# Kernel optimization log

Hardware: AMD Instinct MI355X
Metric: run time of the kernel (lower is better)

## Reference

```python
import jax, jax.numpy as jnp
import numpy as np

NUM_JOINTS = 24
IN_DIM = 256      # PoseMLP hidden_dim (per-joint input feature)
HID = 128         # MLP default hidden_dim
OUT_DIM = 6
B = 16384

def setup_inputs() -> dict:
    key = jax.random.key(0)
    ks = jax.random.split(key, 7)
    s1 = 1.0 / np.sqrt(IN_DIM)   # torch Linear init scale (uniform bound)
    s2 = 1.0 / np.sqrt(HID)
    return {
        "pose_feat": jax.random.normal(ks[0], (B, NUM_JOINTS, IN_DIM), dtype=jnp.float32),
        # stacked per-joint weights: Linear stores W as (out, in); we keep (in, out)
        "W1": jax.random.uniform(ks[1], (NUM_JOINTS, IN_DIM, HID), minval=-s1, maxval=s1, dtype=jnp.float32),
        "b1": jax.random.uniform(ks[2], (NUM_JOINTS, HID), minval=-s1, maxval=s1, dtype=jnp.float32),
        "W2": jax.random.uniform(ks[3], (NUM_JOINTS, HID, HID), minval=-s2, maxval=s2, dtype=jnp.float32),
        "b2": jax.random.uniform(ks[4], (NUM_JOINTS, HID), minval=-s2, maxval=s2, dtype=jnp.float32),
        "W3": jax.random.uniform(ks[5], (NUM_JOINTS, HID, OUT_DIM), minval=-s2, maxval=s2, dtype=jnp.float32),
        "b3": jax.random.uniform(ks[6], (NUM_JOINTS, OUT_DIM), minval=-s2, maxval=s2, dtype=jnp.float32),
    }

def reference(pose_feat, W1, b1, W2, b2, W3, b3):
    # Batched per-joint MLPs (fuses the 24 independent small MLPs into 3 grouped GEMMs)
    h = jax.nn.relu(jnp.einsum('bji,jih->bjh', pose_feat, W1) + b1)  # [B,24,128]
    h = jax.nn.relu(jnp.einsum('bjh,jhk->bjk', h, W2) + b2)          # [B,24,128]
    out = jnp.einsum('bjh,jho->bjo', h, W3) + b3                     # [B,24,6]
    return out
```

## Files before the change

kernel.cpp:

```cpp
#include <hip/hip_runtime.h>
#include <hip/hip_fp16.h>

typedef _Float16 half_t;
typedef __attribute__((ext_vector_type(8))) _Float16 half8;
typedef __attribute__((ext_vector_type(4))) _Float16 half4;
typedef __attribute__((ext_vector_type(4))) float floatx4;

#define NJ 24
#define IN_DIM 256
#define HID 128
#define OUT_DIM 6
#define BATCH 16384

#define NBJ 10
#define GRID (NJ * NBJ)
#define TPJ (BATCH / 16)
#define SLOTS (NBJ * 16)

#define W1_JSTRIDE (8 * 128 * 32)
#define W2_JSTRIDE (4 * 128 * 32)
#define W3_JSTRIDE (16 * 128)
#define WT1_ELEMS (NJ * W1_JSTRIDE)
#define WT2_ELEMS (NJ * W2_JSTRIDE)
#define WT3_ELEMS (NJ * W3_JSTRIDE)
#define WT2_OFF WT1_ELEMS
#define WT3_OFF (WT1_ELEMS + WT2_ELEMS)
#define B3P_BYTE_OFF ((size_t)(WT1_ELEMS + WT2_ELEMS + WT3_ELEMS) * 2)
#define PREP_TOTAL (WT1_ELEMS + WT2_ELEMS + WT3_ELEMS + NJ * 16)

__global__ void posemlp_prep(const float* __restrict__ W1, const float* __restrict__ W2,
                             const float* __restrict__ W3, const float* __restrict__ b3,
                             half_t* __restrict__ wt, float* __restrict__ b3p) {
    int t = blockIdx.x * 256 + threadIdx.x;
    if (t < WT1_ELEMS) {
        int j = t / W1_JSTRIDE, r = t % W1_JSTRIDE;
        int ks = r / 4096, r2 = r % 4096;
        int n = r2 / 32, kk = r2 % 32, k = ks * 32 + kk;
        wt[t] = (half_t)W1[((size_t)j * IN_DIM + k) * HID + n];
    } else if (t < WT2_OFF + WT2_ELEMS) {
        int u = t - WT2_OFF;
        int j = u / W2_JSTRIDE, r = u % W2_JSTRIDE;
        int ks = r / 4096, r2 = r % 4096;
        int n = r2 / 32, kk = r2 % 32, k = ks * 32 + kk;
        wt[t] = (half_t)W2[((size_t)j * HID + k) * HID + n];
    } else if (t < WT3_OFF + WT3_ELEMS) {
        int u = t - WT3_OFF;
        int j = u / W3_JSTRIDE, r = u % W3_JSTRIDE;
        int n = r / 128, k = r % 128;
        wt[t] = (n < OUT_DIM) ? (half_t)W3[((size_t)j * HID + k) * OUT_DIM + n] : (half_t)0.0f;
    } else if (t < PREP_TOTAL) {
        int u = t - WT3_OFF - WT3_ELEMS;
        int j = u / 16, n = u % 16;
        b3p[u] = (n < OUT_DIM) ? b3[j * OUT_DIM + n] : 0.0f;
    }
}

__device__ inline void gll16(const void* g, void* l) {
    __builtin_amdgcn_global_load_lds(
        (const __attribute__((address_space(1))) unsigned int*)g,
        (__attribute__((address_space(3))) unsigned int*)l, 16, 0, 0);
}

__device__ inline half8 lds_read8(const half_t* base, int r, int k) {
    int byte = r * 256 + k * 2;
    byte ^= (r & 7) << 4;
    return *(const half8*)((const char*)base + byte);
}
__device__ inline void lds_write4(half_t* base, int r, int n, half4 v) {
    int byte = r * 256 + n * 2;
    byte ^= (r & 7) << 4;
    *(half4*)((char*)base + byte) = v;
}

__device__ inline half8 cvt8(floatx4 a, floatx4 b) {
    half8 h;
    h[0] = (_Float16)a[0]; h[1] = (_Float16)a[1]; h[2] = (_Float16)a[2]; h[3] = (_Float16)a[3];
    h[4] = (_Float16)b[0]; h[5] = (_Float16)b[1]; h[6] = (_Float16)b[2]; h[7] = (_Float16)b[3];
    return h;
}

__global__ __launch_bounds__(1024) void posemlp_main(
    const float* __restrict__ X, const half_t* __restrict__ wt,
    const float* __restrict__ b1, const float* __restrict__ b2,
    const float* __restrict__ b3p, float* __restrict__ out) {
    __shared__ half_t lds[81920];

    const int bid0 = blockIdx.x;
    const int bid = (bid0 & 7) * 30 + (bid0 >> 3);
    const int j = bid / NBJ, bw = bid % NBJ;
    const int tid = threadIdx.x;
    const int wv = tid >> 6;
    const int l = tid & 63;
    const int lrow = l & 15;
    const int q = l >> 4;

    const half_t* w1j = wt + (size_t)j * W1_JSTRIDE;
    const half_t* w2j = wt + WT2_OFF + (size_t)j * W2_JSTRIDE;
    const half_t* w3j = wt + WT3_OFF + (size_t)j * W3_JSTRIDE;

    const int s = bw * 16 + wv;
    const int nt = (TPJ - s + SLOTS - 1) / SLOTS;

    const float* xg = X + ((size_t)(s * 16 + lrow) * NJ + j) * IN_DIM + q * 8;

    floatx4 px[4][2];
#pragma unroll
    for (int c = 0; c < 4; ++c) {
        px[c][0] = *(const floatx4*)(xg + c * 32);
        px[c][1] = *(const floatx4*)(xg + c * 32 + 4);
    }

    if (wv < 8) {
        const int n = tid >> 2, ss2 = tid & 3;
        const int srcoff = n * 32 + (ss2 ^ ((n >> 1) & 3)) * 8;
#pragma unroll
        for (int c = 0; c < 8; ++c)
            gll16(w1j + c * 4096 + srcoff, &lds[c * 4096 + wv * 512]);
#pragma unroll
        for (int c = 0; c < 4; ++c)
            gll16(w2j + c * 4096 + srcoff, &lds[32768 + c * 4096 + wv * 512]);
    }

    half8 a3[4];
#pragma unroll
    for (int ks = 0; ks < 4; ++ks)
        a3[ks] = *(const half8*)&w3j[lrow * 128 + (ks * 4 + q) * 8];

    half_t* scr = &lds[49152 + wv * 2048];

    __syncthreads();

    for (int i = 0; i < nt; ++i) {
        const size_t nstep = (i + 1 < nt) ? (size_t)(SLOTS * 16) * NJ * IN_DIM : 0;

        floatx4 acc[8] = {};
#pragma unroll
        for (int ks = 0; ks < 8; ++ks) {
            half8 bx = cvt8(px[ks & 3][0], px[ks & 3][1]);
            {
                const float* p = (ks < 4) ? (xg + (ks + 4) * 32)
                                          : (xg + nstep + (ks - 4) * 32);
                px[ks & 3][0] = *(const floatx4*)(p);
                px[ks & 3][1] = *(const floatx4*)(p + 4);
            }
#pragma unroll
            for (int nf = 0; nf < 8; ++nf) {
                const int n = nf * 16 + lrow;
                half8 a = *(const half8*)&lds[ks * 4096 + n * 32 + (q ^ ((n >> 1) & 3)) * 8];
                acc[nf] = __builtin_amdgcn_mfma_f32_16x16x32_f16(a, bx, acc[nf], 0, 0, 0);
            }
        }
        {
            const float* b1j = b1 + j * HID;
#pragma unroll
            for (int nf = 0; nf < 8; ++nf) {
                floatx4 bb = *(const floatx4*)(b1j + nf * 16 + q * 4);
                floatx4 v = acc[nf];
                half4 hv;
#pragma unroll
                for (int e = 0; e < 4; ++e) hv[e] = (_Float16)fmaxf(v[e] + bb[e], 0.0f);
                lds_write4(scr, lrow, nf * 16 + q * 4, hv);
            }
        }

        floatx4 acc2[8] = {};
#pragma unroll
        for (int ks = 0; ks < 4; ++ks) {
            half8 bh = lds_read8(scr, lrow, ks * 32 + q * 8);
#pragma unroll
            for (int nf = 0; nf < 8; ++nf) {
                const int n = nf * 16 + lrow;
                half8 a = *(const half8*)&lds[32768 + ks * 4096 + n * 32 + (q ^ ((n >> 1) & 3)) * 8];
                acc2[nf] = __builtin_amdgcn_mfma_f32_16x16x32_f16(a, bh, acc2[nf], 0, 0, 0);
            }
        }
        {
            const float* b2j = b2 + j * HID;
#pragma unroll
            for (int nf = 0; nf < 8; ++nf) {
                floatx4 bb = *(const floatx4*)(b2j + nf * 16 + q * 4);
                floatx4 v = acc2[nf];
                half4 hv;
#pragma unroll
                for (int e = 0; e < 4; ++e) hv[e] = (_Float16)fmaxf(v[e] + bb[e], 0.0f);
                lds_write4(scr, lrow, nf * 16 + q * 4, hv);
            }
        }

        floatx4 acc3 = {};
#pragma unroll
        for (int ks = 0; ks < 4; ++ks) {
            half8 bh = lds_read8(scr, lrow, ks * 32 + q * 8);
            acc3 = __builtin_amdgcn_mfma_f32_16x16x32_f16(a3[ks], bh, acc3, 0, 0, 0);
        }
        {
            floatx4 bb = *(const floatx4*)(b3p + j * 16 + q * 4);
            const int orow = (s + i * SLOTS) * 16 + lrow;
            float* op = out + ((size_t)orow * NJ + j) * OUT_DIM;
            floatx4 v = acc3;
            if (q == 0) {
                float2 s0 = {v[0] + bb[0], v[1] + bb[1]};
                float2 s1 = {v[2] + bb[2], v[3] + bb[3]};
                *(float2*)(op + 0) = s0;
                *(float2*)(op + 2) = s1;
            } else if (q == 1) {
                float2 s2 = {v[0] + bb[0], v[1] + bb[1]};
                *(float2*)(op + 4) = s2;
            }
        }

        xg += nstep;
    }
}

extern "C" void kernel_launch(void* const* d_in, const int* in_sizes, int n_in,
                              void* d_out, int out_size, void* d_ws, size_t ws_size,
                              hipStream_t stream) {
    const float* X  = (const float*)d_in[0];
    const float* W1 = (const float*)d_in[1];
    const float* b1 = (const float*)d_in[2];
    const float* W2 = (const float*)d_in[3];
    const float* b2 = (const float*)d_in[4];
    const float* W3 = (const float*)d_in[5];
    const float* b3 = (const float*)d_in[6];
    float* out = (float*)d_out;

    half_t* wt = (half_t*)d_ws;
    float* b3p = (float*)((char*)d_ws + B3P_BYTE_OFF);

    int prep_blocks = (PREP_TOTAL + 255) / 256;
    posemlp_prep<<<prep_blocks, 256, 0, stream>>>(W1, W2, W3, b3, wt, b3p);

    posemlp_main<<<GRID, 1024, 0, stream>>>(X, wt, b1, b2, b3p, out);
}
```

Measured before the change: 133.5 us.

## Process 32 rows per wave and transpose weights through LDS in prep

The main kernel now runs 8 waves per block instead of 16, and each wave handles two 16-row MFMA tiles. Every LDS weight fragment it reads feeds two MFMAs, which halves LDS traffic per unit of compute and keeps more X loads in flight per wave. The cost is fewer waves to hide latency and higher register pressure from the doubled accumulators and prefetch buffers. The weight-prep kernel is also rewritten to transpose 32x128 tiles through shared memory, so its global reads and writes are coalesced.

```diff
diff --git a/kernel.cpp b/kernel.cpp
--- a/kernel.cpp
+++ b/kernel.cpp
@@ -14,8 +14,8 @@
 
 #define NBJ 10
 #define GRID (NJ * NBJ)
-#define TPJ (BATCH / 16)
-#define SLOTS (NBJ * 16)
+#define TPJ (BATCH / 32)
+#define SLOTS (NBJ * 8)
 
 #define W1_JSTRIDE (8 * 128 * 32)
 #define W2_JSTRIDE (4 * 128 * 32)
@@ -26,32 +26,56 @@
 #define WT2_OFF WT1_ELEMS
 #define WT3_OFF (WT1_ELEMS + WT2_ELEMS)
 #define B3P_BYTE_OFF ((size_t)(WT1_ELEMS + WT2_ELEMS + WT3_ELEMS) * 2)
-#define PREP_TOTAL (WT1_ELEMS + WT2_ELEMS + WT3_ELEMS + NJ * 16)
-
-__global__ void posemlp_prep(const float* __restrict__ W1, const float* __restrict__ W2,
-                             const float* __restrict__ W3, const float* __restrict__ b3,
-                             half_t* __restrict__ wt, float* __restrict__ b3p) {
-    int t = blockIdx.x * 256 + threadIdx.x;
-    if (t < WT1_ELEMS) {
-        int j = t / W1_JSTRIDE, r = t % W1_JSTRIDE;
-        int ks = r / 4096, r2 = r % 4096;
-        int n = r2 / 32, kk = r2 % 32, k = ks * 32 + kk;
-        wt[t] = (half_t)W1[((size_t)j * IN_DIM + k) * HID + n];
-    } else if (t < WT2_OFF + WT2_ELEMS) {
-        int u = t - WT2_OFF;
-        int j = u / W2_JSTRIDE, r = u % W2_JSTRIDE;
-        int ks = r / 4096, r2 = r % 4096;
-        int n = r2 / 32, kk = r2 % 32, k = ks * 32 + kk;
-        wt[t] = (half_t)W2[((size_t)j * HID + k) * HID + n];
-    } else if (t < WT3_OFF + WT3_ELEMS) {
-        int u = t - WT3_OFF;
-        int j = u / W3_JSTRIDE, r = u % W3_JSTRIDE;
-        int n = r / 128, k = r % 128;
-        wt[t] = (n < OUT_DIM) ? (half_t)W3[((size_t)j * HID + k) * OUT_DIM + n] : (half_t)0.0f;
-    } else if (t < PREP_TOTAL) {
-        int u = t - WT3_OFF - WT3_ELEMS;
-        int j = u / 16, n = u % 16;
-        b3p[u] = (n < OUT_DIM) ? b3[j * OUT_DIM + n] : 0.0f;
+
+__global__ __launch_bounds__(256) void posemlp_prep(
+    const float* __restrict__ W1, const float* __restrict__ W2,
+    const float* __restrict__ W3, const float* __restrict__ b3,
+    half_t* __restrict__ wt, float* __restrict__ b3p) {
+    __shared__ float tile[32][129];
+    const int b = blockIdx.x;
+    const int tid = threadIdx.x;
+
+    if (b < 288) {
+        const float* src;
+        half_t* dst;
+        if (b < 192) {
+            int j = b >> 3, ks = b & 7;
+            src = W1 + ((size_t)j * IN_DIM + ks * 32) * HID;
+            dst = wt + ((size_t)j * 8 + ks) * 4096;
+        } else {
+            int u = b - 192;
+            int j = u >> 2, ks = u & 3;
+            src = W2 + ((size_t)j * HID + ks * 32) * HID;
+            dst = wt + WT2_OFF + ((size_t)j * 4 + ks) * 4096;
+        }
+        {
+            const int n = tid & 127, k2 = tid >> 7;
+#pragma unroll
+            for (int it = 0; it < 16; ++it) {
+                const int k = it * 2 + k2;
+                tile[k][n] = src[(size_t)k * HID + n];
+            }
+        }
+        __syncthreads();
+        {
+            const int kk = tid & 31, nb = tid >> 5;
+#pragma unroll
+            for (int it = 0; it < 16; ++it) {
+                const int n = it * 8 + nb;
+                dst[n * 32 + kk] = (half_t)tile[kk][n];
+            }
+        }
+    } else {
+        for (int idx = tid; idx < NJ * 16 * 128; idx += 256) {
+            int j = idx / 2048, r = idx % 2048;
+            int n = r / 128, k = r % 128;
+            wt[WT3_OFF + idx] = (n < OUT_DIM)
+                ? (half_t)W3[((size_t)j * HID + k) * OUT_DIM + n] : (half_t)0.0f;
+        }
+        for (int idx = tid; idx < NJ * 16; idx += 256) {
+            int j = idx / 16, n = idx % 16;
+            b3p[idx] = (n < OUT_DIM) ? b3[j * OUT_DIM + n] : 0.0f;
+        }
     }
 }
 
@@ -79,7 +103,7 @@
     return h;
 }
 
-__global__ __launch_bounds__(1024) void posemlp_main(
+__global__ __launch_bounds__(512, 2) void posemlp_main(
     const float* __restrict__ X, const half_t* __restrict__ wt,
     const float* __restrict__ b1, const float* __restrict__ b2,
     const float* __restrict__ b3p, float* __restrict__ out) {
@@ -98,19 +122,22 @@
     const half_t* w2j = wt + WT2_OFF + (size_t)j * W2_JSTRIDE;
     const half_t* w3j = wt + WT3_OFF + (size_t)j * W3_JSTRIDE;
 
-    const int s = bw * 16 + wv;
+    const int s = bw * 8 + wv;
     const int nt = (TPJ - s + SLOTS - 1) / SLOTS;
 
-    const float* xg = X + ((size_t)(s * 16 + lrow) * NJ + j) * IN_DIM + q * 8;
-
-    floatx4 px[4][2];
+    const float* xr0 = X + ((size_t)(s * 32 + lrow) * NJ + j) * IN_DIM + q * 8;
+    const float* xr1 = xr0 + (size_t)16 * NJ * IN_DIM;
+
+    floatx4 px[4][2][2];
 #pragma unroll
     for (int c = 0; c < 4; ++c) {
-        px[c][0] = *(const floatx4*)(xg + c * 32);
-        px[c][1] = *(const floatx4*)(xg + c * 32 + 4);
-    }
-
-    if (wv < 8) {
+        px[c][0][0] = *(const floatx4*)(xr0 + c * 32);
+        px[c][0][1] = *(const floatx4*)(xr0 + c * 32 + 4);
+        px[c][1][0] = *(const floatx4*)(xr1 + c * 32);
+        px[c][1][1] = *(const floatx4*)(xr1 + c * 32 + 4);
+    }
+
+    {
         const int n = tid >> 2, ss2 = tid & 3;
         const int srcoff = n * 32 + (ss2 ^ ((n >> 1) & 3)) * 8;
 #pragma unroll
@@ -125,29 +152,36 @@
 #pragma unroll
     for (int ks = 0; ks < 4; ++ks)
         a3[ks] = *(const half8*)&w3j[lrow * 128 + (ks * 4 + q) * 8];
-
-    half_t* scr = &lds[49152 + wv * 2048];
+    const floatx4 bb3 = *(const floatx4*)(b3p + j * 16 + q * 4);
+
+    half_t* scr = &lds[49152 + wv * 4096];
 
     __syncthreads();
 
     for (int i = 0; i < nt; ++i) {
-        const size_t nstep = (i + 1 < nt) ? (size_t)(SLOTS * 16) * NJ * IN_DIM : 0;
-
-        floatx4 acc[8] = {};
+        const size_t nstep = (i + 1 < nt) ? (size_t)(SLOTS * 32) * NJ * IN_DIM : 0;
+
+        floatx4 acc[8][2] = {};
 #pragma unroll
         for (int ks = 0; ks < 8; ++ks) {
-            half8 bx = cvt8(px[ks & 3][0], px[ks & 3][1]);
+            half8 bx0 = cvt8(px[ks & 3][0][0], px[ks & 3][0][1]);
+            half8 bx1 = cvt8(px[ks & 3][1][0], px[ks & 3][1][1]);
             {
-                const float* p = (ks < 4) ? (xg + (ks + 4) * 32)
-                                          : (xg + nstep + (ks - 4) * 32);
-                px[ks & 3][0] = *(const floatx4*)(p);
-                px[ks & 3][1] = *(const floatx4*)(p + 4);
+                const float* p0 = (ks < 4) ? (xr0 + (ks + 4) * 32)
+                                           : (xr0 + nstep + (ks - 4) * 32);
+                const float* p1 = (ks < 4) ? (xr1 + (ks + 4) * 32)
+                                           : (xr1 + nstep + (ks - 4) * 32);
+                px[ks & 3][0][0] = *(const floatx4*)(p0);
+                px[ks & 3][0][1] = *(const floatx4*)(p0 + 4);
+                px[ks & 3][1][0] = *(const floatx4*)(p1);
+                px[ks & 3][1][1] = *(const floatx4*)(p1 + 4);
             }
 #pragma unroll
             for (int nf = 0; nf < 8; ++nf) {
                 const int n = nf * 16 + lrow;
                 half8 a = *(const half8*)&lds[ks * 4096 + n * 32 + (q ^ ((n >> 1) & 3)) * 8];
-                acc[nf] = __builtin_amdgcn_mfma_f32_16x16x32_f16(a, bx, acc[nf], 0, 0, 0);
+                acc[nf][0] = __builtin_amdgcn_mfma_f32_16x16x32_f16(a, bx0, acc[nf][0], 0, 0, 0);
+                acc[nf][1] = __builtin_amdgcn_mfma_f32_16x16x32_f16(a, bx1, acc[nf][1], 0, 0, 0);
             }
         }
         {
@@ -155,23 +189,28 @@
 #pragma unroll
             for (int nf = 0; nf < 8; ++nf) {
                 floatx4 bb = *(const floatx4*)(b1j + nf * 16 + q * 4);
-                floatx4 v = acc[nf];
-                half4 hv;
-#pragma unroll
-                for (int e = 0; e < 4; ++e) hv[e] = (_Float16)fmaxf(v[e] + bb[e], 0.0f);
-                lds_write4(scr, lrow, nf * 16 + q * 4, hv);
-            }
-        }
-
-        floatx4 acc2[8] = {};
+#pragma unroll
+                for (int mf = 0; mf < 2; ++mf) {
+                    floatx4 v = acc[nf][mf];
+                    half4 hv;
+#pragma unroll
+                    for (int e = 0; e < 4; ++e) hv[e] = (_Float16)fmaxf(v[e] + bb[e], 0.0f);
+                    lds_write4(scr, mf * 16 + lrow, nf * 16 + q * 4, hv);
+                }
+            }
+        }
+
+        floatx4 acc2[8][2] = {};
 #pragma unroll
         for (int ks = 0; ks < 4; ++ks) {
-            half8 bh = lds_read8(scr, lrow, ks * 32 + q * 8);
+            half8 bh0 = lds_read8(scr, lrow, ks * 32 + q * 8);
+            half8 bh1 = lds_read8(scr, 16 + lrow, ks * 32 + q * 8);
 #pragma unroll
             for (int nf = 0; nf < 8; ++nf) {
                 const int n = nf * 16 + lrow;
                 half8 a = *(const half8*)&lds[32768 + ks * 4096 + n * 32 + (q ^ ((n >> 1) & 3)) * 8];
-                acc2[nf] = __builtin_amdgcn_mfma_f32_16x16x32_f16(a, bh, acc2[nf], 0, 0, 0);
+                acc2[nf][0] = __builtin_amdgcn_mfma_f32_16x16x32_f16(a, bh0, acc2[nf][0], 0, 0, 0);
+                acc2[nf][1] = __builtin_amdgcn_mfma_f32_16x16x32_f16(a, bh1, acc2[nf][1], 0, 0, 0);
             }
         }
         {
@@ -179,37 +218,46 @@
 #pragma unroll
             for (int nf = 0; nf < 8; ++nf) {
                 floatx4 bb = *(const floatx4*)(b2j + nf * 16 + q * 4);
-                floatx4 v = acc2[nf];
-                half4 hv;
-#pragma unroll
-                for (int e = 0; e < 4; ++e) hv[e] = (_Float16)fmaxf(v[e] + bb[e], 0.0f);
-                lds_write4(scr, lrow, nf * 16 + q * 4, hv);
-            }
-        }
-
-        floatx4 acc3 = {};
+#pragma unroll
+                for (int mf = 0; mf < 2; ++mf) {
+                    floatx4 v = acc2[nf][mf];
+                    half4 hv;
+#pragma unroll
+                    for (int e = 0; e < 4; ++e) hv[e] = (_Float16)fmaxf(v[e] + bb[e], 0.0f);
+                    lds_write4(scr, mf * 16 + lrow, nf * 16 + q * 4, hv);
+                }
+            }
+        }
+
+        floatx4 acc3[2] = {};
 #pragma unroll
         for (int ks = 0; ks < 4; ++ks) {
-            half8 bh = lds_read8(scr, lrow, ks * 32 + q * 8);
-            acc3 = __builtin_amdgcn_mfma_f32_16x16x32_f16(a3[ks], bh, acc3, 0, 0, 0);
-        }
-        {
-            floatx4 bb = *(const floatx4*)(b3p + j * 16 + q * 4);
-            const int orow = (s + i * SLOTS) * 16 + lrow;
-            float* op = out + ((size_t)orow * NJ + j) * OUT_DIM;
-            floatx4 v = acc3;
-            if (q == 0) {
-                float2 s0 = {v[0] + bb[0], v[1] + bb[1]};
-                float2 s1 = {v[2] + bb[2], v[3] + bb[3]};
-                *(float2*)(op + 0) = s0;
-                *(float2*)(op + 2) = s1;
-            } else if (q == 1) {
-                float2 s2 = {v[0] + bb[0], v[1] + bb[1]};
-                *(float2*)(op + 4) = s2;
-            }
-        }
-
-        xg += nstep;
+            half8 bh0 = lds_read8(scr, lrow, ks * 32 + q * 8);
+            half8 bh1 = lds_read8(scr, 16 + lrow, ks * 32 + q * 8);
+            acc3[0] = __builtin_amdgcn_mfma_f32_16x16x32_f16(a3[ks], bh0, acc3[0], 0, 0, 0);
+            acc3[1] = __builtin_amdgcn_mfma_f32_16x16x32_f16(a3[ks], bh1, acc3[1], 0, 0, 0);
+        }
+        {
+            const int trow = (s + i * SLOTS) * 32;
+#pragma unroll
+            for (int mf = 0; mf < 2; ++mf) {
+                const int orow = trow + mf * 16 + lrow;
+                float* op = out + ((size_t)orow * NJ + j) * OUT_DIM;
+                floatx4 v = acc3[mf];
+                if (q == 0) {
+                    float2 s0 = {v[0] + bb3[0], v[1] + bb3[1]};
+                    float2 s1 = {v[2] + bb3[2], v[3] + bb3[3]};
+                    *(float2*)(op + 0) = s0;
+                    *(float2*)(op + 2) = s1;
+                } else if (q == 1) {
+                    float2 s2 = {v[0] + bb3[0], v[1] + bb3[1]};
+                    *(float2*)(op + 4) = s2;
+                }
+            }
+        }
+
+        xr0 += nstep;
+        xr1 += nstep;
     }
 }
 
@@ -228,8 +276,6 @@
     half_t* wt = (half_t*)d_ws;
     float* b3p = (float*)((char*)d_ws + B3P_BYTE_OFF);
 
-    int prep_blocks = (PREP_TOTAL + 255) / 256;
-    posemlp_prep<<<prep_blocks, 256, 0, stream>>>(W1, W2, W3, b3, wt, b3p);
-
-    posemlp_main<<<GRID, 1024, 0, stream>>>(X, wt, b1, b2, b3p, out);
-}
+    posemlp_prep<<<289, 256, 0, stream>>>(W1, W2, W3, b3, wt, b3p);
+    posemlp_main<<<GRID, 512, 0, stream>>>(X, wt, b1, b2, b3p, out);
+}
```

After: 369.0 us. +176.4%, slower.
